# Optimization experiments

Hardware: AMD Instinct MI355X
Metric: run time of the kernel (lower is better)

Reference implementation:

```python
import jax, jax.numpy as jnp
import numpy as np

B, Q, K, C, H, DH, OUT = 32, 512, 512, 256, 8, 32, 256


def setup_inputs() -> dict:
    key = jax.random.key(0)
    ks = jax.random.split(key, 11)
    s = 1.0 / np.sqrt(C)
    return {
        "q_data": jax.random.normal(ks[0], (B, Q, C), jnp.float32),
        "m_data": jax.random.normal(ks[1], (B, K, C), jnp.float32),
        "bias": jax.random.normal(ks[2], (B, 1, Q, K), jnp.float32),
        "nonbatched_bias": jax.random.normal(ks[3], (H, Q, K), jnp.float32),
        "query_w": jax.random.normal(ks[4], (C, H, DH), jnp.float32) * s,
        "key_w": jax.random.normal(ks[5], (C, H, DH), jnp.float32) * s,
        "value_w": jax.random.normal(ks[6], (C, H, DH), jnp.float32) * s,
        "gating_w": jax.random.normal(ks[7], (C, H, DH), jnp.float32) * s,
        "gating_b": jax.random.normal(ks[8], (H, DH), jnp.float32),
        "output_w": jax.random.normal(ks[9], (H, DH, OUT), jnp.float32) * (1.0 / np.sqrt(H * DH)),
        "output_b": jax.random.normal(ks[10], (OUT,), jnp.float32),
    }


def reference(q_data, m_data, bias, nonbatched_bias, query_w, key_w, value_w,
              gating_w, gating_b, output_w, output_b):
    key_dim = query_w.shape[-1]  # per-head key dim
    q = jnp.einsum('bqa,ahc->bqhc', q_data, query_w) * key_dim ** (-0.5)
    k = jnp.einsum('bka,ahc->bkhc', m_data, key_w)
    v = jnp.einsum('bka,ahc->bkhc', m_data, value_w)
    logits = jnp.einsum('bqhc,bkhc->bhqk', q, k) + bias  # [B,H,Q,K]
    logits = logits + nonbatched_bias[None]  # broadcast over batch
    logits = jnp.clip(logits, -1e8, 1e8)
    weights = jax.nn.softmax(logits, axis=-1)
    weighted_avg = jnp.einsum('bhqk,bkhc->bqhc', weights, v)
    gate = jax.nn.sigmoid(jnp.einsum('bqc,chv->bqhv', q_data, gating_w) + gating_b)
    weighted_avg = weighted_avg * gate
    return jnp.einsum('bqhc,hco->bqo', weighted_avg, output_w) + output_b
```

## Files before the change

### kernel.cpp

```cpp
#include <hip/hip_runtime.h>

typedef unsigned short u16;
typedef __attribute__((ext_vector_type(4))) short short4v;
typedef __attribute__((ext_vector_type(8))) short bf16x8;
typedef __attribute__((ext_vector_type(4))) float f32x4;

union Pack8 { u16 h[8]; int4 v; bf16x8 b; };
union Frag8 { bf16x8 v8; short4v h4[2]; };

__device__ __forceinline__ f32x4 mfma16(bf16x8 a, bf16x8 b, f32x4 c) {
    return __builtin_amdgcn_mfma_f32_16x16x32_bf16(a, b, c, 0, 0, 0);
}

__device__ __forceinline__ float bf2f(u16 u) {
    unsigned int x = ((unsigned int)u) << 16;
    return __builtin_bit_cast(float, x);
}

__device__ __forceinline__ u16 f2bf(float f) {
    unsigned int u = __builtin_bit_cast(unsigned int, f);
    u += 0x7FFF + ((u >> 16) & 1);
    return (u16)(u >> 16);
}

__global__ __launch_bounds__(256) void prep_w2(
    const float* __restrict__ qw, const float* __restrict__ kw,
    const float* __restrict__ vw, const float* __restrict__ gw,
    const float* __restrict__ ow,
    u16* __restrict__ wtq, u16* __restrict__ wtm, u16* __restrict__ wto)
{
    const int which = blockIdx.z;
    const float* s = which == 0 ? qw : which == 1 ? kw : which == 2 ? vw
                   : which == 3 ? gw : ow;
    u16* d; int roff;
    if (which == 0)      { d = wtq; roff = 0; }
    else if (which == 3) { d = wtq; roff = 256; }
    else if (which == 1) { d = wtm; roff = 0; }
    else if (which == 2) { d = wtm; roff = 256; }
    else                 { d = wto; roff = 0; }

    const int n0 = blockIdx.x * 64;
    const int c0 = blockIdx.y * 64;

    __shared__ float T[64][68];
    const int rr = threadIdx.x >> 2;
    const int sg = threadIdx.x & 3;
    #pragma unroll
    for (int j = 0; j < 4; ++j) {
        float4 v = *(const float4*)(&s[(size_t)(c0 + rr) * 256 + n0 + sg * 16 + j * 4]);
        *(float4*)(&T[rr][sg * 16 + j * 4]) = v;
    }
    __syncthreads();
    #pragma unroll
    for (int j = 0; j < 4; ++j) {
        union { u16 h[4]; uint2 v; } p;
        #pragma unroll
        for (int e = 0; e < 4; ++e)
            p.h[e] = f2bf(T[sg * 16 + j * 4 + e][rr]);
        *(uint2*)(&d[(size_t)(roff + n0 + rr) * 256 + c0 + sg * 16 + j * 4]) = p.v;
    }
}

__global__ __launch_bounds__(256) void proj128(
    const float* __restrict__ q_data, const float* __restrict__ m_data,
    const u16* __restrict__ wtq, const u16* __restrict__ wtm,
    const float* __restrict__ gating_b,
    u16* __restrict__ qbuf, u16* __restrict__ kbuf,
    u16* __restrict__ vbuf, u16* __restrict__ gbuf)
{
    const int src = blockIdx.z;
    const float* X = src ? m_data : q_data;
    const u16* W = src ? wtm : wtq;

    const int m0 = blockIdx.x * 128;
    const int n0 = blockIdx.y * 128;

    __shared__ __align__(16) u16 SMEM[2][128][72];
    #define Xs (SMEM[0])
    #define Ws (SMEM[1])

    const int tid  = threadIdx.x;
    const int wave = tid >> 6;
    const int wm   = wave >> 1, wn = wave & 1;
    const int lane = tid & 63;
    const int l16  = lane & 15;
    const int quad = lane >> 4;

    const f32x4 kZero = {0.f, 0.f, 0.f, 0.f};
    f32x4 acc[4][4];
    #pragma unroll
    for (int i = 0; i < 4; ++i)
        #pragma unroll
        for (int j = 0; j < 4; ++j) acc[i][j] = kZero;

    const int r  = tid >> 1;
    const int cs = (tid & 1) * 32;

    for (int k0 = 0; k0 < 256; k0 += 64) {
        __syncthreads();
        #pragma unroll
        for (int i = 0; i < 4; ++i) {
            const float4* xp = (const float4*)(&X[(size_t)(m0 + r) * 256 + k0 + cs + i * 8]);
            float4 xa = xp[0], xb = xp[1];
            Pack8 pk;
            pk.h[0] = f2bf(xa.x); pk.h[1] = f2bf(xa.y);
            pk.h[2] = f2bf(xa.z); pk.h[3] = f2bf(xa.w);
            pk.h[4] = f2bf(xb.x); pk.h[5] = f2bf(xb.y);
            pk.h[6] = f2bf(xb.z); pk.h[7] = f2bf(xb.w);
            *(int4*)(&Xs[r][cs + i * 8]) = pk.v;
            *(int4*)(&Ws[r][cs + i * 8]) = *(const int4*)(&W[(size_t)(n0 + r) * 256 + k0 + cs + i * 8]);
        }
        __syncthreads();
        #pragma unroll
        for (int ks = 0; ks < 2; ++ks) {
            bf16x8 a[4], bb[4];
            #pragma unroll
            for (int mf = 0; mf < 4; ++mf)
                a[mf] = *(const bf16x8*)(&Xs[wm * 64 + mf * 16 + l16][ks * 32 + quad * 8]);
            #pragma unroll
            for (int nf = 0; nf < 4; ++nf)
                bb[nf] = *(const bf16x8*)(&Ws[wn * 64 + nf * 16 + l16][ks * 32 + quad * 8]);
            #pragma unroll
            for (int mf = 0; mf < 4; ++mf)
                #pragma unroll
                for (int nf = 0; nf < 4; ++nf)
                    acc[mf][nf] = mfma16(a[mf], bb[nf], acc[mf][nf]);
        }
    }

    const bool second = (n0 >= 256);
    const int b = m0 >> 9, qi0 = m0 & 511;

    __syncthreads();
    u16* T = &SMEM[0][0][0];

    if (src == 1 && second) {
        #pragma unroll
        for (int nf = 0; nf < 4; ++nf) {
            const int nl_ = wn * 64 + nf * 16 + l16;
            #pragma unroll
            for (int mf = 0; mf < 4; ++mf)
                #pragma unroll
                for (int rr = 0; rr < 4; ++rr) {
                    const int ml = wm * 64 + mf * 16 + quad * 4 + rr;
                    T[nl_ * 136 + ml] = f2bf(acc[mf][nf][rr]);
                }
        }
        __syncthreads();
        const int row = tid >> 1, half = tid & 1;
        const int nl = (n0 - 256) + row;
        const int h = nl >> 5, c = nl & 31;
        u16* dst = &vbuf[((size_t)(b * 8 + h) * 32 + c) * 512 + qi0 + half * 64];
        #pragma unroll
        for (int i = 0; i < 8; ++i)
            *(int4*)(&dst[i * 8]) = *(const int4*)(&T[row * 136 + half * 64 + i * 8]);
        return;
    }

    #pragma unroll
    for (int nf = 0; nf < 4; ++nf) {
        const int nl_ = wn * 64 + nf * 16 + l16;
        const int ng = n0 + nl_;
        #pragma unroll
        for (int mf = 0; mf < 4; ++mf) {
            #pragma unroll
            for (int rr = 0; rr < 4; ++rr) {
                const int ml = wm * 64 + mf * 16 + quad * 4 + rr;
                float v = acc[mf][nf][rr];
                u16 val;
                if (src == 0 && !second) {
                    val = f2bf(v * 0.17677669529663689f);
                } else if (src == 0) {
                    val = f2bf(1.0f / (1.0f + __expf(-(v + gating_b[ng - 256]))));
                } else {
                    val = f2bf(v);
                }
                T[ml * 136 + nl_] = val;
            }
        }
    }
    __syncthreads();

    if (src == 0 && second) {
        const int ml = tid >> 1, sub = tid & 1;
        u16* dst = &gbuf[(size_t)(m0 + ml) * 256 + (n0 - 256) + sub * 64];
        #pragma unroll
        for (int i = 0; i < 8; ++i)
            *(int4*)(&dst[i * 8]) = *(const int4*)(&T[ml * 136 + sub * 64 + i * 8]);
    } else {
        u16* D = (src == 0) ? qbuf : kbuf;
        const int hl = tid & 3, h0 = n0 >> 5;
        #pragma unroll
        for (int p = 0; p < 2; ++p) {
            const int ml = p * 64 + (tid >> 2);
            u16* dst = &D[((size_t)(b * 8 + h0 + hl) * 512 + qi0 + ml) * 32];
            #pragma unroll
            for (int i = 0; i < 4; ++i)
                *(int4*)(&dst[i * 8]) = *(const int4*)(&T[ml * 136 + hl * 32 + i * 8]);
        }
    }
    #undef Xs
    #undef Ws
}

__global__ __launch_bounds__(256) void attn_kernel(
    const u16* __restrict__ qbuf, const u16* __restrict__ kbuf,
    const u16* __restrict__ vbuf, const float* __restrict__ bias,
    const float* __restrict__ nb, const u16* __restrict__ gbuf,
    u16* __restrict__ waG)
{
    const int b = blockIdx.z, h = blockIdx.y, q0 = blockIdx.x * 64;
    const int tid  = threadIdx.x;
    const int wave = tid >> 6;
    const int lane = tid & 63;
    const int l16  = lane & 15;
    const int quad = lane >> 4;

    __shared__ __align__(16) u16  Ks[64][40];
    __shared__ __align__(16) u16  Vs[32][72];
    __shared__ __align__(16) float Bs[64][68];
    __shared__ __align__(16) u16  Os[4][16][40];

    const int qrow_base = q0 + wave * 16;
    bf16x8 aQ = *(const bf16x8*)(&qbuf[((b * 8 + h) * 512 + qrow_base + l16) * 32 + quad * 8]);

    const f32x4 kZero = {0.f, 0.f, 0.f, 0.f};
    f32x4 oacc[2] = {kZero, kZero};
    float lsum = 0.f;

    const int krow = tid >> 2, kseg = tid & 3;
    const int vr = tid >> 3,  vseg = tid & 7;
    const int bq = tid >> 2,  bsg = tid & 3;
    const u16* kbase = &kbuf[(size_t)(b * 8 + h) * 512 * 32];
    const u16* vbase = &vbuf[(size_t)(b * 8 + h) * 32 * 512];
    const float* biasb = &bias[((size_t)b * 512 + q0) * 512];
    const float* nbb   = &nb[((size_t)h * 512 + q0) * 512];

    for (int kt = 0; kt < 8; ++kt) {
        const int kk0 = kt * 64;
        __syncthreads();
        *(int4*)(&Ks[krow][kseg * 8]) = *(const int4*)(&kbase[(kk0 + krow) * 32 + kseg * 8]);
        *(int4*)(&Vs[vr][vseg * 8])   = *(const int4*)(&vbase[vr * 512 + kk0 + vseg * 8]);
        #pragma unroll
        for (int i = 0; i < 4; ++i) {
            const int c = bsg * 16 + i * 4;
            float4 bv = *(const float4*)(&biasb[(size_t)bq * 512 + kk0 + c]);
            float4 nv = *(const float4*)(&nbb[(size_t)bq * 512 + kk0 + c]);
            float4 s = make_float4(bv.x + nv.x, bv.y + nv.y, bv.z + nv.z, bv.w + nv.w);
            *(float4*)(&Bs[bq][c]) = s;
        }
        __syncthreads();

        float p[4][4];
        #pragma unroll
        for (int kn = 0; kn < 4; ++kn) {
            f32x4 cb = *(const f32x4*)(&Bs[wave * 16 + l16][kn * 16 + quad * 4]);
            bf16x8 aK = *(const bf16x8*)(&Ks[kn * 16 + l16][quad * 8]);
            f32x4 st = mfma16(aK, aQ, cb);
            #pragma unroll
            for (int rr = 0; rr < 4; ++rr) {
                float pv = __expf(st[rr]);
                p[kn][rr] = pv;
                lsum += pv;
            }
        }

        #pragma unroll
        for (int pr = 0; pr < 2; ++pr) {
            Frag8 bP;
            #pragma unroll
            for (int rr = 0; rr < 4; ++rr) {
                bP.h4[0][rr] = (short)f2bf(p[2 * pr][rr]);
                bP.h4[1][rr] = (short)f2bf(p[2 * pr + 1][rr]);
            }
            #pragma unroll
            for (int ct = 0; ct < 2; ++ct) {
                Frag8 aV;
                aV.h4[0] = *(const short4v*)(&Vs[ct * 16 + l16][pr * 32 + quad * 4]);
                aV.h4[1] = *(const short4v*)(&Vs[ct * 16 + l16][pr * 32 + 16 + quad * 4]);
                oacc[ct] = mfma16(aV.v8, bP.v8, oacc[ct]);
            }
        }
    }

    lsum += __shfl_xor(lsum, 16, 64);
    lsum += __shfl_xor(lsum, 32, 64);
    const float linv = 1.0f / lsum;

    #pragma unroll
    for (int ct = 0; ct < 2; ++ct)
        #pragma unroll
        for (int rr = 0; rr < 4; ++rr)
            Os[wave][l16][ct * 16 + quad * 4 + rr] = f2bf(oacc[ct][rr] * linv);

    __asm__ __volatile__("" ::: "memory");

    const int orow = lane >> 2, osg = lane & 3;
    Pack8 ov, gv;
    ov.v = *(const int4*)(&Os[wave][orow][osg * 8]);
    size_t gidx = ((size_t)(b * 512 + q0 + wave * 16 + orow)) * 256 + h * 32 + osg * 8;
    gv.v = *(const int4*)(&gbuf[gidx]);
    Pack8 outv;
    #pragma unroll
    for (int i = 0; i < 8; ++i)
        outv.h[i] = f2bf(bf2f(ov.h[i]) * bf2f(gv.h[i]));
    *(int4*)(&waG[gidx]) = outv.v;
}

__global__ __launch_bounds__(256) void out_gemm128(
    const u16* __restrict__ waG, const u16* __restrict__ wto,
    const float* __restrict__ out_b, float* __restrict__ out)
{
    const int m0 = blockIdx.x * 128;
    const int n0 = blockIdx.y * 128;

    __shared__ __align__(16) u16 Xs[128][72];
    __shared__ __align__(16) u16 Ws[128][72];

    const int tid  = threadIdx.x;
    const int wave = tid >> 6;
    const int wm   = wave >> 1, wn = wave & 1;
    const int lane = tid & 63;
    const int l16  = lane & 15;
    const int quad = lane >> 4;

    const f32x4 kZero = {0.f, 0.f, 0.f, 0.f};
    f32x4 acc[4][4];
    #pragma unroll
    for (int i = 0; i < 4; ++i)
        #pragma unroll
        for (int j = 0; j < 4; ++j) acc[i][j] = kZero;

    const int r  = tid >> 1;
    const int cs = (tid & 1) * 32;

    for (int k0 = 0; k0 < 256; k0 += 64) {
        __syncthreads();
        #pragma unroll
        for (int i = 0; i < 4; ++i) {
            *(int4*)(&Xs[r][cs + i * 8]) = *(const int4*)(&waG[(size_t)(m0 + r) * 256 + k0 + cs + i * 8]);
            *(int4*)(&Ws[r][cs + i * 8]) = *(const int4*)(&wto[(size_t)(n0 + r) * 256 + k0 + cs + i * 8]);
        }
        __syncthreads();
        #pragma unroll
        for (int ks = 0; ks < 2; ++ks) {
            bf16x8 a[4], bb[4];
            #pragma unroll
            for (int mf = 0; mf < 4; ++mf)
                a[mf] = *(const bf16x8*)(&Xs[wm * 64 + mf * 16 + l16][ks * 32 + quad * 8]);
            #pragma unroll
            for (int nf = 0; nf < 4; ++nf)
                bb[nf] = *(const bf16x8*)(&Ws[wn * 64 + nf * 16 + l16][ks * 32 + quad * 8]);
            #pragma unroll
            for (int mf = 0; mf < 4; ++mf)
                #pragma unroll
                for (int nf = 0; nf < 4; ++nf)
                    acc[mf][nf] = mfma16(a[mf], bb[nf], acc[mf][nf]);
        }
    }

    #pragma unroll
    for (int nf = 0; nf < 4; ++nf) {
        const int n = n0 + wn * 64 + nf * 16 + l16;
        const float ob = out_b[n];
        #pragma unroll
        for (int mf = 0; mf < 4; ++mf) {
            #pragma unroll
            for (int rr = 0; rr < 4; ++rr) {
                const int m = m0 + wm * 64 + mf * 16 + quad * 4 + rr;
                out[(size_t)m * 256 + n] = acc[mf][nf][rr] + ob;
            }
        }
    }
}

extern "C" void kernel_launch(void* const* d_in, const int* in_sizes, int n_in,
                              void* d_out, int out_size, void* d_ws, size_t ws_size,
                              hipStream_t stream)
{
    const float* q_data = (const float*)d_in[0];
    const float* m_data = (const float*)d_in[1];
    const float* bias   = (const float*)d_in[2];
    const float* nb     = (const float*)d_in[3];
    const float* qw     = (const float*)d_in[4];
    const float* kw     = (const float*)d_in[5];
    const float* vw     = (const float*)d_in[6];
    const float* gw     = (const float*)d_in[7];
    const float* gb     = (const float*)d_in[8];
    const float* ow     = (const float*)d_in[9];
    const float* ob     = (const float*)d_in[10];

    char* ws = (char*)d_ws;
    u16* wtq  = (u16*)ws;
    u16* wtm  = wtq + 131072;
    u16* wto  = wtm + 131072;
    u16* qbuf = wto + 65536;
    u16* kbuf = qbuf + 4194304;
    u16* vbuf = kbuf + 4194304;
    u16* gbuf = vbuf + 4194304;
    u16* waG  = gbuf + 4194304;

    prep_w2<<<dim3(4, 4, 5), 256, 0, stream>>>(qw, kw, vw, gw, ow, wtq, wtm, wto);
    proj128<<<dim3(128, 4, 2), 256, 0, stream>>>(q_data, m_data, wtq, wtm, gb,
                                                 qbuf, kbuf, vbuf, gbuf);
    attn_kernel<<<dim3(8, 8, 32), 256, 0, stream>>>(qbuf, kbuf, vbuf, bias, nb,
                                                    gbuf, waG);
    out_gemm128<<<dim3(128, 2), 256, 0, stream>>>(waG, wto, ob, (float*)d_out);
}
```

Baseline: 224.7 us.

## Prefetch next K/V/bias tile into registers during attention compute

```diff
diff --git a/kernel.cpp b/kernel.cpp
--- a/kernel.cpp
+++ b/kernel.cpp
@@ -216,10 +216,9 @@
     const int l16  = lane & 15;
     const int quad = lane >> 4;
 
-    __shared__ __align__(16) u16  Ks[64][40];
-    __shared__ __align__(16) u16  Vs[32][72];
-    __shared__ __align__(16) float Bs[64][68];
-    __shared__ __align__(16) u16  Os[4][16][40];
+    __shared__ __align__(16) u16   Ks[64][40];
+    __shared__ __align__(16) u16   Vs[32][72];
+    __shared__ __align__(16) float Bs[4][16][68];
 
     const int qrow_base = q0 + wave * 16;
     bf16x8 aQ = *(const bf16x8*)(&qbuf[((b * 8 + h) * 512 + qrow_base + l16) * 32 + quad * 8]);
@@ -230,31 +229,48 @@
 
     const int krow = tid >> 2, kseg = tid & 3;
     const int vr = tid >> 3,  vseg = tid & 7;
-    const int bq = tid >> 2,  bsg = tid & 3;
+    const int br = lane >> 2, bc = (lane & 3) * 16;
     const u16* kbase = &kbuf[(size_t)(b * 8 + h) * 512 * 32];
     const u16* vbase = &vbuf[(size_t)(b * 8 + h) * 32 * 512];
-    const float* biasb = &bias[((size_t)b * 512 + q0) * 512];
-    const float* nbb   = &nb[((size_t)h * 512 + q0) * 512];
+    const float* bl = &bias[((size_t)b * 512 + qrow_base + br) * 512];
+    const float* nl = &nb[((size_t)h * 512 + qrow_base + br) * 512];
+
+    int4 kreg = *(const int4*)(&kbase[krow * 32 + kseg * 8]);
+    int4 vreg = *(const int4*)(&vbase[vr * 512 + vseg * 8]);
+    float4 bbp[4], nnp[4];
+    #pragma unroll
+    for (int i = 0; i < 4; ++i) {
+        bbp[i] = *(const float4*)(&bl[bc + i * 4]);
+        nnp[i] = *(const float4*)(&nl[bc + i * 4]);
+    }
 
     for (int kt = 0; kt < 8; ++kt) {
-        const int kk0 = kt * 64;
-        __syncthreads();
-        *(int4*)(&Ks[krow][kseg * 8]) = *(const int4*)(&kbase[(kk0 + krow) * 32 + kseg * 8]);
-        *(int4*)(&Vs[vr][vseg * 8])   = *(const int4*)(&vbase[vr * 512 + kk0 + vseg * 8]);
+        __syncthreads();
+        *(int4*)(&Ks[krow][kseg * 8]) = kreg;
+        *(int4*)(&Vs[vr][vseg * 8])   = vreg;
         #pragma unroll
         for (int i = 0; i < 4; ++i) {
-            const int c = bsg * 16 + i * 4;
-            float4 bv = *(const float4*)(&biasb[(size_t)bq * 512 + kk0 + c]);
-            float4 nv = *(const float4*)(&nbb[(size_t)bq * 512 + kk0 + c]);
-            float4 s = make_float4(bv.x + nv.x, bv.y + nv.y, bv.z + nv.z, bv.w + nv.w);
-            *(float4*)(&Bs[bq][c]) = s;
-        }
-        __syncthreads();
+            float4 s = make_float4(bbp[i].x + nnp[i].x, bbp[i].y + nnp[i].y,
+                                   bbp[i].z + nnp[i].z, bbp[i].w + nnp[i].w);
+            *(float4*)(&Bs[wave][br][bc + i * 4]) = s;
+        }
+        __syncthreads();
+
+        if (kt < 7) {
+            const int kk1 = (kt + 1) * 64;
+            kreg = *(const int4*)(&kbase[(kk1 + krow) * 32 + kseg * 8]);
+            vreg = *(const int4*)(&vbase[vr * 512 + kk1 + vseg * 8]);
+            #pragma unroll
+            for (int i = 0; i < 4; ++i) {
+                bbp[i] = *(const float4*)(&bl[kk1 + bc + i * 4]);
+                nnp[i] = *(const float4*)(&nl[kk1 + bc + i * 4]);
+            }
+        }
 
         float p[4][4];
         #pragma unroll
         for (int kn = 0; kn < 4; ++kn) {
-            f32x4 cb = *(const f32x4*)(&Bs[wave * 16 + l16][kn * 16 + quad * 4]);
+            f32x4 cb = *(const f32x4*)(&Bs[wave][l16][kn * 16 + quad * 4]);
             bf16x8 aK = *(const bf16x8*)(&Ks[kn * 16 + l16][quad * 8]);
             f32x4 st = mfma16(aK, aQ, cb);
             #pragma unroll
@@ -287,17 +303,18 @@
     lsum += __shfl_xor(lsum, 32, 64);
     const float linv = 1.0f / lsum;
 
+    u16* OsW = (u16*)&Bs[wave][0][0];
     #pragma unroll
     for (int ct = 0; ct < 2; ++ct)
         #pragma unroll
         for (int rr = 0; rr < 4; ++rr)
-            Os[wave][l16][ct * 16 + quad * 4 + rr] = f2bf(oacc[ct][rr] * linv);
+            OsW[l16 * 40 + ct * 16 + quad * 4 + rr] = f2bf(oacc[ct][rr] * linv);
 
     __asm__ __volatile__("" ::: "memory");
 
     const int orow = lane >> 2, osg = lane & 3;
     Pack8 ov, gv;
-    ov.v = *(const int4*)(&Os[wave][orow][osg * 8]);
+    ov.v = *(const int4*)(&OsW[orow * 40 + osg * 8]);
     size_t gidx = ((size_t)(b * 512 + q0 + wave * 16 + orow)) * 256 + h * 32 + osg * 8;
     gv.v = *(const int4*)(&gbuf[gidx]);
     Pack8 outv;
```

Measured after the change: 218.6 us. 2.7% less time.
